# Kernel tuning notes

Hardware: AMD Instinct MI355X
Metric: run time of the kernel (lower is better)

Reference implementation:

```python
import jax, jax.numpy as jnp
import numpy as np
from jax import lax

B, T, N, F, K = 8, 16, 1024, 128, 4


def setup_inputs() -> dict:
    key = jax.random.key(0)
    k1, k2, k3, k4 = jax.random.split(key, 4)
    x = jax.random.normal(k1, (B, T, N, F), dtype=jnp.float32)
    # shift operator scaled so its spectral radius is ~1 (stable powers L^1..L^K)
    L = jax.random.normal(k2, (N, N), dtype=jnp.float32) / jnp.sqrt(jnp.float32(N))
    # xavier_uniform with relu gain: limit = gain * sqrt(6/(fan_in+fan_out))
    gain = jnp.sqrt(jnp.float32(2.0))
    lim = gain * jnp.sqrt(6.0 / (F + F))
    W = jax.random.uniform(k3, (K, F, F), dtype=jnp.float32, minval=-lim, maxval=lim)
    H = jax.random.uniform(k4, (K, F, F), dtype=jnp.float32, minval=-lim, maxval=lim)
    return {"x": x, "L": L, "W": W, "H": H}


def reference(x, L, W, H):
    """Recurrent graph-polynomial filter.

    h_t = relu( sum_{k=0}^{K-1} L^{k+1} @ (x_t @ W[k] + h_{t-1} @ H[k]) ), h_{-1}=0.
    Matches the torch loop where alpha_k starts at L and is multiplied by L each tap.
    """
    Kt = W.shape[0]
    # powers L^1 .. L^K, stacked [K, N, N]
    pows = [L]
    for _ in range(1, Kt):
        pows.append(pows[-1] @ L)
    Lp = jnp.stack(pows)

    def step(h, x_t):
        # x_t, h: [B, N, F]
        s = jnp.einsum('bnf,kfg->kbng', x_t, W) + jnp.einsum('bnf,kfg->kbng', h, H)
        z = jnp.einsum('knm,kbmg->bng', Lp, s)
        h_new = jax.nn.relu(z)
        return h_new, h_new

    xT = jnp.swapaxes(x, 0, 1)          # [T, B, N, F]
    h0 = jnp.zeros_like(x[:, 0])        # [B, N, F]
    _, outs = lax.scan(step, h0, xT)    # [T, B, N, F]
    return jnp.swapaxes(outs, 0, 1)     # [B, T, N, F]
```

## Files before the change

kernel.cpp:

```cpp
#include <hip/hip_runtime.h>
#include <stdint.h>


typedef __bf16 bf16_t;
typedef __bf16 bf16x4 __attribute__((ext_vector_type(4)));
typedef __bf16 bf16x8 __attribute__((ext_vector_type(8)));
typedef float  f32x4  __attribute__((ext_vector_type(4)));
typedef float  f32x16 __attribute__((ext_vector_type(16)));

__device__ __forceinline__ void gload_lds16(const void* g, void* l) {
    __builtin_amdgcn_global_load_lds(
        (const __attribute__((address_space(1))) void*)g,
        (__attribute__((address_space(3))) void*)l,
        16, 0, 0);
}


__global__ void k_convert_x(const float* __restrict__ xin,
                            bf16_t* __restrict__ xb, int n4) {
    int i = blockIdx.x * 256 + threadIdx.x;
    int stride = gridDim.x * 256;
    for (; i < n4; i += stride) {
        float4 v = reinterpret_cast<const float4*>(xin)[i];
        bf16x4 o = { (bf16_t)v.x, (bf16_t)v.y, (bf16_t)v.z, (bf16_t)v.w };
        reinterpret_cast<bf16x4*>(xb)[i] = o;
    }
}

__global__ void k_setup_L(const float* __restrict__ L,
                          bf16_t* __restrict__ Lcat,
                          bf16_t* __restrict__ Lt) {
    int idx = blockIdx.x * 256 + threadIdx.x;
    int n = idx >> 10, m = idx & 1023;
    float v = L[idx];
    Lcat[n * 4096 + m] = (bf16_t)v;
    Lt[m * 1024 + n]   = (bf16_t)v;
}

__global__ void k_setup_WH(const float* __restrict__ W,
                           const float* __restrict__ H,
                           bf16_t* __restrict__ WHT) {
    int idx = blockIdx.x * 256 + threadIdx.x;
    int k = idx >> 14, f = (idx >> 7) & 127, g = idx & 127;
    WHT[(k * 128 + g) * 256 + f]       = (bf16_t)W[idx];
    WHT[(k * 128 + g) * 256 + 128 + f] = (bf16_t)H[idx];
}


__global__ __launch_bounds__(256)
void k_combine(const float* __restrict__ Zp,
               bf16_t* __restrict__ h, float* __restrict__ out, int t) {
    int i = blockIdx.x * 256 + threadIdx.x;
    int n  = i >> 8;
    int cg = (i & 255) * 4;
    size_t o = (size_t)n * 1024 + cg;
    float4 v0 = *reinterpret_cast<const float4*>(Zp + o);
    float4 v1 = *reinterpret_cast<const float4*>(Zp + 1048576 + o);
    float4 v2 = *reinterpret_cast<const float4*>(Zp + 2097152 + o);
    float4 v3 = *reinterpret_cast<const float4*>(Zp + 3145728 + o);
    float4 s;
    s.x = fmaxf(v0.x + v1.x + v2.x + v3.x, 0.f);
    s.y = fmaxf(v0.y + v1.y + v2.y + v3.y, 0.f);
    s.z = fmaxf(v0.z + v1.z + v2.z + v3.z, 0.f);
    s.w = fmaxf(v0.w + v1.w + v2.w + v3.w, 0.f);
    int b = cg >> 7, g = cg & 127;
    size_t ho = (size_t)b * 131072 + (size_t)n * 128 + g;
    bf16x4 hb = { (bf16_t)s.x, (bf16_t)s.y, (bf16_t)s.z, (bf16_t)s.w };
    *reinterpret_cast<bf16x4*>(h + ho) = hb;
    *reinterpret_cast<float4*>(out + (size_t)b * 2097152
                                   + (size_t)t * 131072
                                   + (size_t)n * 128 + g) = s;
}

template<int BM, int BN, int GX, int GY, int GZ, int KTOT,
         int EPI, int BADDR, int ZK, int DEC>
__device__ __forceinline__
void gemm_body(const bf16_t* __restrict__ A, int lda,
               const bf16_t* __restrict__ BT, int ldbt,
               const bf16_t* __restrict__ B2,
               bf16_t* __restrict__ Cb, float* __restrict__ Cf,
               int ldc, int t)
{
    constexpr int BK = 64;
    constexpr int WM = BM / 2, WN = BN / 2;
    constexpr int MF = WM / 32, NF = WN / 32;
    constexpr int NT = KTOT / BK;
    constexpr int NWG = GX * GY * GZ;
    constexpr int ACH = BM * 8;
    constexpr int BCH = BN * 8;
    constexpr int LPT = (ACH + BCH) / 256;

    __shared__ __align__(16) bf16_t As[3][BM * BK];
    __shared__ __align__(16) bf16_t Bs[3][BN * BK];

    const int tid  = threadIdx.x;
    const int lane = tid & 63;
    const int wave = tid >> 6;
    const int wm = wave >> 1, wn = wave & 1;

    const int id  = blockIdx.x;
    const int swz = (id & 7) * (NWG / 8) + (id >> 3);
    int bx, by, bz;
    if (DEC == 0) {
        bx = swz % GX; by = (swz / GX) % GY; bz = swz / (GX * GY);
    } else {
        by = swz % GY; bz = (swz / GY) % GZ; bx = swz / (GY * GZ);
    }

    const int m0 = by * BM;
    const int c0 = bx * BN;
    const int kb_ = bz;

    const bf16_t* Ap = (EPI == 1) ? (A + kb_ * 128 * 256) : A;

    f32x16 acc[MF][NF] = {};

    auto stage = [&](int bufi, int kt) {
        const int q0 = kt * BK + (ZK > 0 ? kb_ * ZK : 0);
        #pragma unroll
        for (int i = 0; i < ACH / 256; ++i) {
            int chunk = i * 256 + tid;
            int off = chunk * 16;
            int row = off >> 7;
            int kel = ((off ^ ((row & 7) << 4)) & 127) >> 1;
            const bf16_t* src = Ap + (size_t)(m0 + row) * lda + (q0 + kel);
            gload_lds16(src, (char*)(&As[bufi][0]) + off);
        }
        #pragma unroll
        for (int i = 0; i < BCH / 256; ++i) {
            int chunk = i * 256 + tid;
            int off = chunk * 16;
            int row = off >> 7;
            int kel = ((off ^ ((row & 7) << 4)) & 127) >> 1;
            int c = c0 + row;
            const bf16_t* src;
            if (BADDR == 0) {
                src = BT + (size_t)c * ldbt + (q0 + kel);
            } else {
                int f = q0 + kel;
                if (q0 < 128) {
                    src = BT + (size_t)(c >> 10) * 2097152
                             + (size_t)t * 131072
                             + (size_t)(c & 1023) * 128 + f;
                } else {
                    src = B2 + (size_t)c * 128 + (f - 128);
                }
            }
            gload_lds16(src, (char*)(&Bs[bufi][0]) + off);
        }
    };

    stage(0, 0);
    stage(1, 1);

    for (int kt = 0; kt < NT; ++kt) {
        if (kt < NT - 1) {
            if constexpr (LPT == 4)
                asm volatile("s_waitcnt vmcnt(4)" ::: "memory");
            else if constexpr (LPT == 6)
                asm volatile("s_waitcnt vmcnt(6)" ::: "memory");
            else
                asm volatile("s_waitcnt vmcnt(8)" ::: "memory");
        } else {
            asm volatile("s_waitcnt vmcnt(0)" ::: "memory");
        }
        __builtin_amdgcn_s_barrier();
        __builtin_amdgcn_sched_barrier(0);

        if (kt + 2 < NT) stage((kt + 2) % 3, kt + 2);

        const int cur = kt % 3;
        #pragma unroll
        for (int kk = 0; kk < 4; ++kk) {
            bf16x8 af[MF], bfr[NF];
            const int klane = kk * 32 + (lane >> 5) * 16;
            #pragma unroll
            for (int mf = 0; mf < MF; ++mf) {
                int row = wm * WM + mf * 32 + (lane & 31);
                int bo = (row * 128 + klane) ^ ((row & 7) << 4);
                af[mf] = *reinterpret_cast<const bf16x8*>(
                             (const char*)(&As[cur][0]) + bo);
            }
            #pragma unroll
            for (int nf = 0; nf < NF; ++nf) {
                int row = wn * WN + nf * 32 + (lane & 31);
                int bo = (row * 128 + klane) ^ ((row & 7) << 4);
                bfr[nf] = *reinterpret_cast<const bf16x8*>(
                              (const char*)(&Bs[cur][0]) + bo);
            }
            #pragma unroll
            for (int mf = 0; mf < MF; ++mf)
                #pragma unroll
                for (int nf = 0; nf < NF; ++nf)
                    acc[mf][nf] = __builtin_amdgcn_mfma_f32_32x32x16_bf16(
                        af[mf], bfr[nf], acc[mf][nf], 0, 0, 0);
        }
        __builtin_amdgcn_sched_barrier(0);
    }

    #pragma unroll
    for (int mf = 0; mf < MF; ++mf) {
        #pragma unroll
        for (int nf = 0; nf < NF; ++nf) {
            f32x16 v = acc[mf][nf];
            int col   = c0 + wn * WN + nf * 32 + (lane & 31);
            int rbase = m0 + wm * WM + mf * 32 + 4 * (lane >> 5);
            #pragma unroll
            for (int r = 0; r < 16; ++r) {
                int row = rbase + (r & 3) + 8 * (r >> 2);
                float val = v[r];
                if (EPI == 0) {
                    Cb[(size_t)row * ldc + col] = (bf16_t)val;
                } else if (EPI == 1) {
                    Cb[(size_t)(col >> 10) * 524288 + (size_t)row * 4096
                       + (size_t)kb_ * 1024 + (col & 1023)] = (bf16_t)val;
                } else if (EPI == 2) {
                    val = fmaxf(val, 0.f);
                    int b = col >> 7, g = col & 127;
                    Cb[(size_t)b * 131072 + (size_t)row * 128 + g] = (bf16_t)val;
                    Cf[(size_t)b * 2097152 + (size_t)t * 131072
                       + (size_t)row * 128 + g] = val;
                } else {
                    Cf[(size_t)kb_ * 1048576 + (size_t)row * 1024 + col] = val;
                }
            }
        }
    }
}


__global__ __launch_bounds__(256)
void k_chain(const bf16_t* __restrict__ A, const bf16_t* __restrict__ BT,
             bf16_t* __restrict__ Cb) {
    gemm_body<64, 64, 16, 16, 1, 1024, 0, 0, 0, 0>(
        A, 4096, BT, 1024, nullptr, Cb, nullptr, 4096, 0);
}

__global__ __launch_bounds__(256)
void k_feat(const bf16_t* __restrict__ WHT, const bf16_t* __restrict__ xb,
            const bf16_t* __restrict__ h, bf16_t* __restrict__ Sbuf, int t) {
    gemm_body<64, 128, 64, 2, 4, 256, 1, 1, 0, 1>(
        WHT, 256, xb, 0, h, Sbuf, nullptr, 0, t);
}

__global__ __launch_bounds__(256)
void k_graph(const bf16_t* __restrict__ Lcat, const bf16_t* __restrict__ Sbuf,
             float* __restrict__ Zp) {
    gemm_body<128, 64, 16, 8, 4, 1024, 3, 0, 1024, 0>(
        Lcat, 4096, Sbuf, 4096, nullptr, nullptr, Zp, 0, 0);
}

__global__ __launch_bounds__(256)
void k_graph_ns(const bf16_t* __restrict__ Lcat, const bf16_t* __restrict__ Sbuf,
                bf16_t* __restrict__ h, float* __restrict__ out, int t) {
    gemm_body<128, 128, 8, 8, 1, 4096, 2, 0, 0, 0>(
        Lcat, 4096, Sbuf, 4096, nullptr, h, out, 0, t);
}


extern "C" void kernel_launch(void* const* d_in, const int* in_sizes, int n_in,
                              void* d_out, int out_size, void* d_ws, size_t ws_size,
                              hipStream_t stream) {
    const float* x = (const float*)d_in[0];
    const float* L = (const float*)d_in[1];
    const float* W = (const float*)d_in[2];
    const float* H = (const float*)d_in[3];
    float* out = (float*)d_out;

    char* ws = (char*)d_ws;
    bf16_t* xb   = (bf16_t*)(ws);
    bf16_t* Lcat = (bf16_t*)(ws + 33554432);
    bf16_t* Lt   = (bf16_t*)(ws + 41943040);
    bf16_t* WHT  = (bf16_t*)(ws + 44040192);
    bf16_t* Sbuf = (bf16_t*)(ws + 44302336);
    bf16_t* h    = (bf16_t*)(ws + 52690944);
    float*  Zp   = (float*) (ws + 54788096);
    if (ws_size < 54788096u) return;
    const bool bigws = (ws_size >= 71565312u);

    hipMemsetAsync(h, 0, 2097152, stream);
    k_convert_x<<<4096, 256, 0, stream>>>(x, xb, 16777216 / 4);
    k_setup_L <<<4096, 256, 0, stream>>>(L, Lcat, Lt);
    k_setup_WH<<<256, 256, 0, stream>>>(W, H, WHT);

    for (int p = 1; p < 4; ++p) {
        k_chain<<<256, 256, 0, stream>>>(Lcat + (p - 1) * 1024, Lt,
                                         Lcat + p * 1024);
    }

    for (int t = 0; t < 16; ++t) {
        k_feat<<<512, 256, 0, stream>>>(WHT, xb, h, Sbuf, t);
        if (bigws) {
            k_graph<<<512, 256, 0, stream>>>(Lcat, Sbuf, Zp);
            k_combine<<<1024, 256, 0, stream>>>(Zp, h, out, t);
        } else {
            k_graph_ns<<<64, 256, 0, stream>>>(Lcat, Sbuf, h, out, t);
        }
    }
}
```

Before: 519.4 us.

## Replace split-K graph GEMM plus combine with single 64x64-tile fused GEMM

Removes the split-K graph GEMM path that wrote four fp32 partial buffers and a separate combine kernel. Each timestep now runs one non-split graph GEMM with 64x64 tiles across 256 workgroups, applying ReLU and writing h and out directly in the epilogue. This drops the partial-sum round trip through memory and one launch per step. In exchange each workgroup walks the full K=4096 reduction serially with smaller tiles, so there is less B-tile reuse than the 128-wide tiles.

```diff
diff --git a/kernel.cpp b/kernel.cpp
--- a/kernel.cpp
+++ b/kernel.cpp
@@ -44,32 +44,6 @@
     int k = idx >> 14, f = (idx >> 7) & 127, g = idx & 127;
     WHT[(k * 128 + g) * 256 + f]       = (bf16_t)W[idx];
     WHT[(k * 128 + g) * 256 + 128 + f] = (bf16_t)H[idx];
-}
-
-
-__global__ __launch_bounds__(256)
-void k_combine(const float* __restrict__ Zp,
-               bf16_t* __restrict__ h, float* __restrict__ out, int t) {
-    int i = blockIdx.x * 256 + threadIdx.x;
-    int n  = i >> 8;
-    int cg = (i & 255) * 4;
-    size_t o = (size_t)n * 1024 + cg;
-    float4 v0 = *reinterpret_cast<const float4*>(Zp + o);
-    float4 v1 = *reinterpret_cast<const float4*>(Zp + 1048576 + o);
-    float4 v2 = *reinterpret_cast<const float4*>(Zp + 2097152 + o);
-    float4 v3 = *reinterpret_cast<const float4*>(Zp + 3145728 + o);
-    float4 s;
-    s.x = fmaxf(v0.x + v1.x + v2.x + v3.x, 0.f);
-    s.y = fmaxf(v0.y + v1.y + v2.y + v3.y, 0.f);
-    s.z = fmaxf(v0.z + v1.z + v2.z + v3.z, 0.f);
-    s.w = fmaxf(v0.w + v1.w + v2.w + v3.w, 0.f);
-    int b = cg >> 7, g = cg & 127;
-    size_t ho = (size_t)b * 131072 + (size_t)n * 128 + g;
-    bf16x4 hb = { (bf16_t)s.x, (bf16_t)s.y, (bf16_t)s.z, (bf16_t)s.w };
-    *reinterpret_cast<bf16x4*>(h + ho) = hb;
-    *reinterpret_cast<float4*>(out + (size_t)b * 2097152
-                                   + (size_t)t * 131072
-                                   + (size_t)n * 128 + g) = s;
 }
 
 template<int BM, int BN, int GX, int GY, int GZ, int KTOT,
@@ -214,14 +188,12 @@
                 } else if (EPI == 1) {
                     Cb[(size_t)(col >> 10) * 524288 + (size_t)row * 4096
                        + (size_t)kb_ * 1024 + (col & 1023)] = (bf16_t)val;
-                } else if (EPI == 2) {
+                } else {
                     val = fmaxf(val, 0.f);
                     int b = col >> 7, g = col & 127;
                     Cb[(size_t)b * 131072 + (size_t)row * 128 + g] = (bf16_t)val;
                     Cf[(size_t)b * 2097152 + (size_t)t * 131072
                        + (size_t)row * 128 + g] = val;
-                } else {
-                    Cf[(size_t)kb_ * 1048576 + (size_t)row * 1024 + col] = val;
                 }
             }
         }
@@ -244,16 +216,9 @@
 }
 
 __global__ __launch_bounds__(256)
-void k_graph(const bf16_t* __restrict__ Lcat, const bf16_t* __restrict__ Sbuf,
-             float* __restrict__ Zp) {
-    gemm_body<128, 64, 16, 8, 4, 1024, 3, 0, 1024, 0>(
-        Lcat, 4096, Sbuf, 4096, nullptr, nullptr, Zp, 0, 0);
-}
-
-__global__ __launch_bounds__(256)
-void k_graph_ns(const bf16_t* __restrict__ Lcat, const bf16_t* __restrict__ Sbuf,
-                bf16_t* __restrict__ h, float* __restrict__ out, int t) {
-    gemm_body<128, 128, 8, 8, 1, 4096, 2, 0, 0, 0>(
+void k_graph64(const bf16_t* __restrict__ Lcat, const bf16_t* __restrict__ Sbuf,
+               bf16_t* __restrict__ h, float* __restrict__ out, int t) {
+    gemm_body<64, 64, 16, 16, 1, 4096, 2, 0, 0, 0>(
         Lcat, 4096, Sbuf, 4096, nullptr, h, out, 0, t);
 }
 
@@ -274,9 +239,7 @@
     bf16_t* WHT  = (bf16_t*)(ws + 44040192);
     bf16_t* Sbuf = (bf16_t*)(ws + 44302336);
     bf16_t* h    = (bf16_t*)(ws + 52690944);
-    float*  Zp   = (float*) (ws + 54788096);
     if (ws_size < 54788096u) return;
-    const bool bigws = (ws_size >= 71565312u);
 
     hipMemsetAsync(h, 0, 2097152, stream);
     k_convert_x<<<4096, 256, 0, stream>>>(x, xb, 16777216 / 4);
@@ -290,11 +253,6 @@
 
     for (int t = 0; t < 16; ++t) {
         k_feat<<<512, 256, 0, stream>>>(WHT, xb, h, Sbuf, t);
-        if (bigws) {
-            k_graph<<<512, 256, 0, stream>>>(Lcat, Sbuf, Zp);
-            k_combine<<<1024, 256, 0, stream>>>(Zp, h, out, t);
-        } else {
-            k_graph_ns<<<64, 256, 0, stream>>>(Lcat, Sbuf, h, out, t);
-        }
-    }
-}
+        k_graph64<<<256, 256, 0, stream>>>(Lcat, Sbuf, h, out, t);
+    }
+}
```

Result: slower. 874.1 us (+68.3%).
